# Kernel tuning notes

Hardware: AMD Instinct MI355X
Metric: run time of the kernel (lower is better)

## Reference

```python
import jax, jax.numpy as jnp
import numpy as np

N = 8192
IN_F = 128
OUT_F = 128
ALPHA = 0.2  # LeakyReLU negative slope
NEG_INF = -9e15


def setup_inputs() -> dict:
    key = jax.random.key(0)
    k1, k2, k3, k4 = jax.random.split(key, 4)
    h = jax.random.normal(k1, (N, IN_F), dtype=jnp.float32)
    adj = jax.random.randint(k2, (N, N), 0, 2, dtype=jnp.int32)
    # nn.Linear(in, out, bias=False).weight is (out, in); store as (in, out) for h @ W
    W = jax.random.normal(k3, (IN_F, OUT_F), dtype=jnp.float32) * (1.0 / np.sqrt(IN_F))
    # a: (2*out_features, 1), xavier_uniform with gain=1.414
    limit = 1.414 * np.sqrt(6.0 / (2 * OUT_F + 1))
    a = jax.random.uniform(k4, (2 * OUT_F, 1), dtype=jnp.float32, minval=-limit, maxval=limit)
    return {"h": h, "adj": adj, "W": W, "a": a}


def reference(h, adj, W, a):
    Wh = h @ W  # (N, OUT_F)
    a1 = a[:OUT_F, 0]   # score contribution from source node i
    a2 = a[OUT_F:, 0]   # score contribution from target node j
    # e_ij = leakyrelu(Wh_i . a1 + Wh_j . a2) -- avoids the O(N^2 * 2F) concat
    s1 = Wh @ a1  # (N,)
    s2 = Wh @ a2  # (N,)
    e = jax.nn.leaky_relu(s1[:, None] + s2[None, :], negative_slope=ALPHA)  # (N, N)
    masked = jnp.where(adj > 0, e, NEG_INF)
    attention = jax.nn.softmax(masked, axis=1)  # (N, N)
    # dropout is a no-op in eval mode
    h_prime = attention @ Wh  # (N, OUT_F)
    return jax.nn.elu(h_prime)  # concat=True -> ELU
```

## Files before the change

### kernel.cpp

```cpp
#include <hip/hip_runtime.h>
#include <cstdint>
#include <cstddef>


#define NROW 8192
#define FDIM 128

typedef _Float16 f16;
typedef f16 f16x8 __attribute__((ext_vector_type(8)));
typedef float f32x4 __attribute__((ext_vector_type(4)));
typedef float f32x16 __attribute__((ext_vector_type(16)));

#define WS_WHT 0u
#define WS_BP  (2u*1024u*1024u)
#define WS_S12 (4u*1024u*1024u)
#define WS_RC  (WS_S12 + 64u*1024u)
#define WS_EF  (WS_RC + 128u*1024u)
#define WS_M2  (WS_EF + 64u*1024u)
#define WS_PWS (WS_M2 + 4u*1024u)

__global__ __launch_bounds__(256) void k1_wh(const float* __restrict__ h,
                                             const float* __restrict__ W,
                                             f16* __restrict__ WhT,
                                             f16* __restrict__ Bp,
                                             unsigned* __restrict__ M2key) {
  __shared__ float hT[128 * 36];
  const int t = (int)threadIdx.x;
  const int rb = (int)blockIdx.x * 32;
  if (blockIdx.x == 0 && t == 0) *M2key = 0u;
  const f32x4* hv = (const f32x4*)(h + (size_t)rb * FDIM);
#pragma unroll
  for (int i = 0; i < 4; ++i) {
    int fidx = t + i * 256;
    f32x4 v = hv[fidx];
    int e0 = fidx * 4;
    int r = e0 >> 7, k = e0 & 127;
    hT[(k + 0) * 36 + r] = v[0];
    hT[(k + 1) * 36 + r] = v[1];
    hT[(k + 2) * 36 + r] = v[2];
    hT[(k + 3) * 36 + r] = v[3];
  }
  __syncthreads();
  const int f = t & 127, rh = t >> 7;
  f32x4 z = {0.f, 0.f, 0.f, 0.f};
  f32x4 acc0 = z, acc1 = z, acc2 = z, acc3 = z;
  for (int k = 0; k < 128; ++k) {
    float w = W[k * FDIM + f];
    const f32x4* hp = (const f32x4*)(hT + k * 36 + rh * 16);
    acc0 += hp[0] * w;
    acc1 += hp[1] * w;
    acc2 += hp[2] * w;
    acc3 += hp[3] * w;
  }
  union { f16 hx[16]; uint4 u[2]; } pk;
#pragma unroll
  for (int q = 0; q < 4; ++q) {
    pk.hx[0 + q]  = (f16)acc0[q];
    pk.hx[4 + q]  = (f16)acc1[q];
    pk.hx[8 + q]  = (f16)acc2[q];
    pk.hx[12 + q] = (f16)acc3[q];
  }
  uint4* dst = (uint4*)(WhT + (size_t)f * NROW + rb + rh * 16);
  dst[0] = pk.u[0];
  dst[1] = pk.u[1];
  f16* bdst = Bp + ((size_t)((blockIdx.x * 2 + rh) * 4 + (f >> 5)) * 64 + (f & 31)) * 8;
  *(uint4*)bdst = pk.u[0];
  *(uint4*)(bdst + 256) = pk.u[1];
}

__global__ __launch_bounds__(256) void k1b_s(const f16* __restrict__ WhT,
                                             const float* __restrict__ a,
                                             float2* __restrict__ s12,
                                             unsigned* __restrict__ M2key) {
  __shared__ float part[2][4][64];
  const int l = (int)threadIdx.x & 63;
  const int fc = (int)threadIdx.x >> 6;
  const int r = (int)blockIdx.x * 64 + l;
  float s1 = 0.f, s2 = 0.f;
  for (int f = fc * 32; f < fc * 32 + 32; ++f) {
    float w = (float)WhT[(size_t)f * NROW + r];
    s1 = fmaf(w, a[f], s1);
    s2 = fmaf(w, a[128 + f], s2);
  }
  part[0][fc][l] = s1;
  part[1][fc][l] = s2;
  __syncthreads();
  if (fc == 0) {
    s1 = part[0][0][l] + part[0][1][l] + part[0][2][l] + part[0][3][l];
    s2 = part[1][0][l] + part[1][1][l] + part[1][2][l] + part[1][3][l];
    s12[r] = make_float2(s1, s2);
    float mx = s2;
#pragma unroll
    for (int off = 32; off; off >>= 1) mx = fmaxf(mx, __shfl_xor(mx, off, 64));
    if (l == 0) {
      unsigned key = __float_as_uint(mx);
      key = (key & 0x80000000u) ? ~key : (key | 0x80000000u);
      atomicMax(M2key, key);
    }
  }
}

__global__ __launch_bounds__(256) void k1c_prep(const float2* __restrict__ s12,
                                                const unsigned* __restrict__ M2key,
                                                float4* __restrict__ RC,
                                                float2* __restrict__ EF) {
  int j = (int)blockIdx.x * 256 + (int)threadIdx.x;
  unsigned key = *M2key;
  float M2 = (key & 0x80000000u) ? __uint_as_float(key ^ 0x80000000u)
                                 : __uint_as_float(~key);
  float2 s = s12[j];
  float c = s.x + M2;
  c = fmaxf(c, 0.2f * c);
  RC[j] = make_float4(__expf(-s.x), __expf(s.x - c), __expf(0.2f * s.x - c), 0.f);
  EF[j] = make_float2(__expf(s.y), __expf(0.2f * s.y));
}

__global__ __launch_bounds__(256) void k2_main(const int* __restrict__ adj,
                                               const f16* __restrict__ Bp,
                                               const float4* __restrict__ RC,
                                               const float* __restrict__ EF,
                                               float* __restrict__ Pws,
                                               float* __restrict__ Dws,
                                               int jspan) {
  const int tid = (int)threadIdx.x;
  const int L = tid & 63, w = tid >> 6;
  const int wid = (int)blockIdx.x * 4 + w;
  const int rg = wid & 255;
  const int c = wid >> 8;
  const int rb = rg * 32;
  const int m = L & 31, kb = L >> 5;
  const int row = rb + m;
  const int j0 = c * jspan;
  const int niter = jspan >> 5;

  const float4 rc = RC[row];
  const float tau = rc.x, kap1 = rc.y, kap2 = rc.z;

  const int* ap = adj + (size_t)row * NROW + j0 + kb * 8;
  const f32x4* ep = (const f32x4*)(EF + 2 * (j0 + kb * 8));
  const f16* bp = Bp + (size_t)(j0 >> 4) * 2048 + L * 8;

  int4 A0 = *(const int4*)ap;
  int4 A1 = *(const int4*)(ap + 4);
  int4 A2 = *(const int4*)(ap + 16);
  int4 A3 = *(const int4*)(ap + 20);
  f32x4 E0 = ep[0], E1 = ep[1], E2 = ep[2], E3 = ep[3];
  f32x4 E4 = ep[8], E5 = ep[9], E6 = ep[10], E7 = ep[11];

  f32x16 zz = {0.f};
  f32x16 acc[4] = {zz, zz, zz, zz};
  float dloc = 0.f;

  for (int it = 0; it < niter; ++it) {
    const f16* bt = bp + (size_t)it * 4096;
    f16x8 B00 = *(const f16x8*)(bt);
    f16x8 B01 = *(const f16x8*)(bt + 512);
    f16x8 B02 = *(const f16x8*)(bt + 1024);
    f16x8 B03 = *(const f16x8*)(bt + 1536);
    f16x8 B10 = *(const f16x8*)(bt + 2048);
    f16x8 B11 = *(const f16x8*)(bt + 2560);
    f16x8 B12 = *(const f16x8*)(bt + 3072);
    f16x8 B13 = *(const f16x8*)(bt + 3584);

    f16x8 af0, af1;
    {
      float p;
      p = (E0[0] > tau) ? E0[0] * kap1 : E0[1] * kap2; p = (A0.x > 0) ? p : 0.f; dloc += p; af0[0] = (f16)p;
      p = (E0[2] > tau) ? E0[2] * kap1 : E0[3] * kap2; p = (A0.y > 0) ? p : 0.f; dloc += p; af0[1] = (f16)p;
      p = (E1[0] > tau) ? E1[0] * kap1 : E1[1] * kap2; p = (A0.z > 0) ? p : 0.f; dloc += p; af0[2] = (f16)p;
      p = (E1[2] > tau) ? E1[2] * kap1 : E1[3] * kap2; p = (A0.w > 0) ? p : 0.f; dloc += p; af0[3] = (f16)p;
      p = (E2[0] > tau) ? E2[0] * kap1 : E2[1] * kap2; p = (A1.x > 0) ? p : 0.f; dloc += p; af0[4] = (f16)p;
      p = (E2[2] > tau) ? E2[2] * kap1 : E2[3] * kap2; p = (A1.y > 0) ? p : 0.f; dloc += p; af0[5] = (f16)p;
      p = (E3[0] > tau) ? E3[0] * kap1 : E3[1] * kap2; p = (A1.z > 0) ? p : 0.f; dloc += p; af0[6] = (f16)p;
      p = (E3[2] > tau) ? E3[2] * kap1 : E3[3] * kap2; p = (A1.w > 0) ? p : 0.f; dloc += p; af0[7] = (f16)p;
      p = (E4[0] > tau) ? E4[0] * kap1 : E4[1] * kap2; p = (A2.x > 0) ? p : 0.f; dloc += p; af1[0] = (f16)p;
      p = (E4[2] > tau) ? E4[2] * kap1 : E4[3] * kap2; p = (A2.y > 0) ? p : 0.f; dloc += p; af1[1] = (f16)p;
      p = (E5[0] > tau) ? E5[0] * kap1 : E5[1] * kap2; p = (A2.z > 0) ? p : 0.f; dloc += p; af1[2] = (f16)p;
      p = (E5[2] > tau) ? E5[2] * kap1 : E5[3] * kap2; p = (A2.w > 0) ? p : 0.f; dloc += p; af1[3] = (f16)p;
      p = (E6[0] > tau) ? E6[0] * kap1 : E6[1] * kap2; p = (A3.x > 0) ? p : 0.f; dloc += p; af1[4] = (f16)p;
      p = (E6[2] > tau) ? E6[2] * kap1 : E6[3] * kap2; p = (A3.y > 0) ? p : 0.f; dloc += p; af1[5] = (f16)p;
      p = (E7[0] > tau) ? E7[0] * kap1 : E7[1] * kap2; p = (A3.z > 0) ? p : 0.f; dloc += p; af1[6] = (f16)p;
      p = (E7[2] > tau) ? E7[2] * kap1 : E7[3] * kap2; p = (A3.w > 0) ? p : 0.f; dloc += p; af1[7] = (f16)p;
    }

    int adv = (it < niter - 1) ? 1 : 0;
    ap += adv * 32;
    ep += adv * 16;
    A0 = *(const int4*)ap;
    A1 = *(const int4*)(ap + 4);
    A2 = *(const int4*)(ap + 16);
    A3 = *(const int4*)(ap + 20);
    E0 = ep[0]; E1 = ep[1]; E2 = ep[2]; E3 = ep[3];
    E4 = ep[8]; E5 = ep[9]; E6 = ep[10]; E7 = ep[11];

    acc[0] = __builtin_amdgcn_mfma_f32_32x32x16_f16(af0, B00, acc[0], 0, 0, 0);
    acc[1] = __builtin_amdgcn_mfma_f32_32x32x16_f16(af0, B01, acc[1], 0, 0, 0);
    acc[2] = __builtin_amdgcn_mfma_f32_32x32x16_f16(af0, B02, acc[2], 0, 0, 0);
    acc[3] = __builtin_amdgcn_mfma_f32_32x32x16_f16(af0, B03, acc[3], 0, 0, 0);
    acc[0] = __builtin_amdgcn_mfma_f32_32x32x16_f16(af1, B10, acc[0], 0, 0, 0);
    acc[1] = __builtin_amdgcn_mfma_f32_32x32x16_f16(af1, B11, acc[1], 0, 0, 0);
    acc[2] = __builtin_amdgcn_mfma_f32_32x32x16_f16(af1, B12, acc[2], 0, 0, 0);
    acc[3] = __builtin_amdgcn_mfma_f32_32x32x16_f16(af1, B13, acc[3], 0, 0, 0);
  }

  dloc += __shfl_xor(dloc, 32, 64);
  if (L < 32) Dws[(size_t)c * NROW + row] = dloc;

  float* P = Pws + ((size_t)c * NROW + rb) * FDIM + (L & 31);
#pragma unroll
  for (int nt = 0; nt < 4; ++nt) {
#pragma unroll
    for (int reg = 0; reg < 16; ++reg) {
      int rr = (reg & 3) + 8 * (reg >> 2) + 4 * kb;
      P[(size_t)rr * FDIM + nt * 32] = acc[nt][reg];
    }
  }
}

__global__ __launch_bounds__(256) void k3_comb(const float* __restrict__ Pws,
                                               const float* __restrict__ Dws,
                                               float* __restrict__ out, int S) {
  int g = (int)blockIdx.x * 256 + (int)threadIdx.x;
  int r = g >> 5, f4 = g & 31;
  f32x4 s = {0.f, 0.f, 0.f, 0.f};
  float den = 0.f;
  for (int c2 = 0; c2 < S; ++c2) {
    s += *(const f32x4*)(Pws + ((size_t)c2 * NROW + r) * FDIM + f4 * 4);
    den += Dws[(size_t)c2 * NROW + r];
  }
  float inv = 1.0f / den;
  f32x4 o;
#pragma unroll
  for (int e = 0; e < 4; ++e) {
    float x = s[e] * inv;
    o[e] = x > 0.f ? x : expm1f(x);
  }
  *(f32x4*)(out + (size_t)r * FDIM + f4 * 4) = o;
}

extern "C" void kernel_launch(void* const* d_in, const int* in_sizes, int n_in,
                              void* d_out, int out_size, void* d_ws, size_t ws_size,
                              hipStream_t stream) {
  const float* h = (const float*)d_in[0];
  const int* adj = (const int*)d_in[1];
  const float* W = (const float*)d_in[2];
  const float* a = (const float*)d_in[3];
  float* out = (float*)d_out;
  char* ws = (char*)d_ws;
  f16* WhT = (f16*)(ws + WS_WHT);
  f16* Bp = (f16*)(ws + WS_BP);
  float2* s12 = (float2*)(ws + WS_S12);
  float4* RC = (float4*)(ws + WS_RC);
  float2* EF = (float2*)(ws + WS_EF);
  unsigned* M2 = (unsigned*)(ws + WS_M2);

  const size_t partial_bytes = (size_t)NROW * FDIM * 4;
  int S = (ws_size >= WS_PWS + 8 * partial_bytes + 8 * NROW * 4) ? 8 : 2;
  float* Pws = (float*)(ws + WS_PWS);
  float* Dws = (float*)(ws + WS_PWS + (size_t)S * partial_bytes);
  int jspan = NROW / S;

  k1_wh<<<dim3(256), dim3(256), 0, stream>>>(h, W, WhT, Bp, M2);
  k1b_s<<<dim3(128), dim3(256), 0, stream>>>(WhT, a, s12, M2);
  k1c_prep<<<dim3(32), dim3(256), 0, stream>>>(s12, M2, RC, EF);
  k2_main<<<dim3(64 * S), dim3(256), 0, stream>>>(adj, Bp, RC, (const float*)EF, Pws, Dws, jspan);
  k3_comb<<<dim3(1024), dim3(256), 0, stream>>>(Pws, Dws, out, S);
}
```

Before: 449.8 us.

## Switch attention GEMM to 16x16x32 MFMA tiles with deeper adjacency prefetch

The main kernel now gives each wave 16 rows instead of 32 and uses 16x16x32 MFMA, so twice as many waves run and there are more in flight to hide the adjacency stream from HBM. The Wh operand layout written by k1_wh is changed to match the new fragment shape. Adjacency loads are prefetched four iterations ahead to raise memory-level parallelism. The LeakyReLU branch on tau is replaced by fmaxf of the two exponential products, which removes the tau table. The cost is that each B fragment is now reused over only 16 rows, which doubles B traffic from L2.

```diff
diff --git a/kernel.cpp b/kernel.cpp
--- a/kernel.cpp
+++ b/kernel.cpp
@@ -9,13 +9,12 @@
 typedef _Float16 f16;
 typedef f16 f16x8 __attribute__((ext_vector_type(8)));
 typedef float f32x4 __attribute__((ext_vector_type(4)));
-typedef float f32x16 __attribute__((ext_vector_type(16)));
 
 #define WS_WHT 0u
 #define WS_BP  (2u*1024u*1024u)
 #define WS_S12 (4u*1024u*1024u)
-#define WS_RC  (WS_S12 + 64u*1024u)
-#define WS_EF  (WS_RC + 128u*1024u)
+#define WS_K12 (WS_S12 + 64u*1024u)
+#define WS_EF  (WS_K12 + 64u*1024u)
 #define WS_M2  (WS_EF + 64u*1024u)
 #define WS_PWS (WS_M2 + 4u*1024u)
 
@@ -63,9 +62,10 @@
   uint4* dst = (uint4*)(WhT + (size_t)f * NROW + rb + rh * 16);
   dst[0] = pk.u[0];
   dst[1] = pk.u[1];
-  f16* bdst = Bp + ((size_t)((blockIdx.x * 2 + rh) * 4 + (f >> 5)) * 64 + (f & 31)) * 8;
+  f16* bdst = Bp + (size_t)blockIdx.x * 4096 + (size_t)(f >> 4) * 512
+                 + (size_t)(2 * rh) * 128 + (size_t)(f & 15) * 8;
   *(uint4*)bdst = pk.u[0];
-  *(uint4*)(bdst + 256) = pk.u[1];
+  *(uint4*)(bdst + 128) = pk.u[1];
 }
 
 __global__ __launch_bounds__(256) void k1b_s(const f16* __restrict__ WhT,
@@ -102,7 +102,7 @@
 
 __global__ __launch_bounds__(256) void k1c_prep(const float2* __restrict__ s12,
                                                 const unsigned* __restrict__ M2key,
-                                                float4* __restrict__ RC,
+                                                float2* __restrict__ K12,
                                                 float2* __restrict__ EF) {
   int j = (int)blockIdx.x * 256 + (int)threadIdx.x;
   unsigned key = *M2key;
@@ -111,13 +111,13 @@
   float2 s = s12[j];
   float c = s.x + M2;
   c = fmaxf(c, 0.2f * c);
-  RC[j] = make_float4(__expf(-s.x), __expf(s.x - c), __expf(0.2f * s.x - c), 0.f);
+  K12[j] = make_float2(__expf(s.x - c), __expf(0.2f * s.x - c));
   EF[j] = make_float2(__expf(s.y), __expf(0.2f * s.y));
 }
 
 __global__ __launch_bounds__(256) void k2_main(const int* __restrict__ adj,
                                                const f16* __restrict__ Bp,
-                                               const float4* __restrict__ RC,
+                                               const float2* __restrict__ K12,
                                                const float* __restrict__ EF,
                                                float* __restrict__ Pws,
                                                float* __restrict__ Dws,
@@ -125,94 +125,96 @@
   const int tid = (int)threadIdx.x;
   const int L = tid & 63, w = tid >> 6;
   const int wid = (int)blockIdx.x * 4 + w;
-  const int rg = wid & 255;
-  const int c = wid >> 8;
-  const int rb = rg * 32;
-  const int m = L & 31, kb = L >> 5;
+  const int rg = wid & 511;
+  const int c = wid >> 9;
+  const int rb = rg * 16;
+  const int m = L & 15, kq = L >> 4;
   const int row = rb + m;
   const int j0 = c * jspan;
   const int niter = jspan >> 5;
 
-  const float4 rc = RC[row];
-  const float tau = rc.x, kap1 = rc.y, kap2 = rc.z;
-
-  const int* ap = adj + (size_t)row * NROW + j0 + kb * 8;
-  const f32x4* ep = (const f32x4*)(EF + 2 * (j0 + kb * 8));
-  const f16* bp = Bp + (size_t)(j0 >> 4) * 2048 + L * 8;
-
-  int4 A0 = *(const int4*)ap;
-  int4 A1 = *(const int4*)(ap + 4);
-  int4 A2 = *(const int4*)(ap + 16);
-  int4 A3 = *(const int4*)(ap + 20);
-  f32x4 E0 = ep[0], E1 = ep[1], E2 = ep[2], E3 = ep[3];
-  f32x4 E4 = ep[8], E5 = ep[9], E6 = ep[10], E7 = ep[11];
-
-  f32x16 zz = {0.f};
-  f32x16 acc[4] = {zz, zz, zz, zz};
+  const float2 kk = K12[row];
+  const float kap1 = kk.x, kap2 = kk.y;
+
+  const int* ap = adj + (size_t)row * NROW + j0 + kq * 8;
+  const float* ep = EF ? (EF + 2 * (size_t)(j0 + kq * 8)) : EF;
+  const f16* bp = Bp + (size_t)(j0 >> 5) * 4096 + (size_t)L * 8;
+
+  int4 A[4][2];
+#pragma unroll
+  for (int s = 0; s < 4; ++s) {
+    A[s][0] = *(const int4*)(ap + s * 32);
+    A[s][1] = *(const int4*)(ap + s * 32 + 4);
+  }
+  f32x4 E[4];
+#pragma unroll
+  for (int q = 0; q < 4; ++q) E[q] = *(const f32x4*)(ep + q * 4);
+
+  f32x4 z = {0.f, 0.f, 0.f, 0.f};
+  f32x4 acc[8] = {z, z, z, z, z, z, z, z};
   float dloc = 0.f;
 
-  for (int it = 0; it < niter; ++it) {
-    const f16* bt = bp + (size_t)it * 4096;
-    f16x8 B00 = *(const f16x8*)(bt);
-    f16x8 B01 = *(const f16x8*)(bt + 512);
-    f16x8 B02 = *(const f16x8*)(bt + 1024);
-    f16x8 B03 = *(const f16x8*)(bt + 1536);
-    f16x8 B10 = *(const f16x8*)(bt + 2048);
-    f16x8 B11 = *(const f16x8*)(bt + 2560);
-    f16x8 B12 = *(const f16x8*)(bt + 3072);
-    f16x8 B13 = *(const f16x8*)(bt + 3584);
-
-    f16x8 af0, af1;
-    {
-      float p;
-      p = (E0[0] > tau) ? E0[0] * kap1 : E0[1] * kap2; p = (A0.x > 0) ? p : 0.f; dloc += p; af0[0] = (f16)p;
-      p = (E0[2] > tau) ? E0[2] * kap1 : E0[3] * kap2; p = (A0.y > 0) ? p : 0.f; dloc += p; af0[1] = (f16)p;
-      p = (E1[0] > tau) ? E1[0] * kap1 : E1[1] * kap2; p = (A0.z > 0) ? p : 0.f; dloc += p; af0[2] = (f16)p;
-      p = (E1[2] > tau) ? E1[2] * kap1 : E1[3] * kap2; p = (A0.w > 0) ? p : 0.f; dloc += p; af0[3] = (f16)p;
-      p = (E2[0] > tau) ? E2[0] * kap1 : E2[1] * kap2; p = (A1.x > 0) ? p : 0.f; dloc += p; af0[4] = (f16)p;
-      p = (E2[2] > tau) ? E2[2] * kap1 : E2[3] * kap2; p = (A1.y > 0) ? p : 0.f; dloc += p; af0[5] = (f16)p;
-      p = (E3[0] > tau) ? E3[0] * kap1 : E3[1] * kap2; p = (A1.z > 0) ? p : 0.f; dloc += p; af0[6] = (f16)p;
-      p = (E3[2] > tau) ? E3[2] * kap1 : E3[3] * kap2; p = (A1.w > 0) ? p : 0.f; dloc += p; af0[7] = (f16)p;
-      p = (E4[0] > tau) ? E4[0] * kap1 : E4[1] * kap2; p = (A2.x > 0) ? p : 0.f; dloc += p; af1[0] = (f16)p;
-      p = (E4[2] > tau) ? E4[2] * kap1 : E4[3] * kap2; p = (A2.y > 0) ? p : 0.f; dloc += p; af1[1] = (f16)p;
-      p = (E5[0] > tau) ? E5[0] * kap1 : E5[1] * kap2; p = (A2.z > 0) ? p : 0.f; dloc += p; af1[2] = (f16)p;
-      p = (E5[2] > tau) ? E5[2] * kap1 : E5[3] * kap2; p = (A2.w > 0) ? p : 0.f; dloc += p; af1[3] = (f16)p;
-      p = (E6[0] > tau) ? E6[0] * kap1 : E6[1] * kap2; p = (A3.x > 0) ? p : 0.f; dloc += p; af1[4] = (f16)p;
-      p = (E6[2] > tau) ? E6[2] * kap1 : E6[3] * kap2; p = (A3.y > 0) ? p : 0.f; dloc += p; af1[5] = (f16)p;
-      p = (E7[0] > tau) ? E7[0] * kap1 : E7[1] * kap2; p = (A3.z > 0) ? p : 0.f; dloc += p; af1[6] = (f16)p;
-      p = (E7[2] > tau) ? E7[2] * kap1 : E7[3] * kap2; p = (A3.w > 0) ? p : 0.f; dloc += p; af1[7] = (f16)p;
+  for (int ii = 0; ii < niter; ii += 4) {
+#pragma unroll
+    for (int s = 0; s < 4; ++s) {
+      const int it = ii + s;
+      const f16* bt = bp + (size_t)it * 4096;
+      f16x8 B0 = *(const f16x8*)(bt);
+      f16x8 B1 = *(const f16x8*)(bt + 512);
+      f16x8 B2 = *(const f16x8*)(bt + 1024);
+      f16x8 B3 = *(const f16x8*)(bt + 1536);
+      f16x8 B4 = *(const f16x8*)(bt + 2048);
+      f16x8 B5 = *(const f16x8*)(bt + 2560);
+      f16x8 B6 = *(const f16x8*)(bt + 3072);
+      f16x8 B7 = *(const f16x8*)(bt + 3584);
+
+      f16x8 af;
+      {
+        const int4 a0 = A[s][0], a1 = A[s][1];
+        float p;
+        p = fmaxf(E[0][0] * kap1, E[0][1] * kap2); p = (a0.x > 0) ? p : 0.f; dloc += p; af[0] = (f16)p;
+        p = fmaxf(E[0][2] * kap1, E[0][3] * kap2); p = (a0.y > 0) ? p : 0.f; dloc += p; af[1] = (f16)p;
+        p = fmaxf(E[1][0] * kap1, E[1][1] * kap2); p = (a0.z > 0) ? p : 0.f; dloc += p; af[2] = (f16)p;
+        p = fmaxf(E[1][2] * kap1, E[1][3] * kap2); p = (a0.w > 0) ? p : 0.f; dloc += p; af[3] = (f16)p;
+        p = fmaxf(E[2][0] * kap1, E[2][1] * kap2); p = (a1.x > 0) ? p : 0.f; dloc += p; af[4] = (f16)p;
+        p = fmaxf(E[2][2] * kap1, E[2][3] * kap2); p = (a1.y > 0) ? p : 0.f; dloc += p; af[5] = (f16)p;
+        p = fmaxf(E[3][0] * kap1, E[3][1] * kap2); p = (a1.z > 0) ? p : 0.f; dloc += p; af[6] = (f16)p;
+        p = fmaxf(E[3][2] * kap1, E[3][3] * kap2); p = (a1.w > 0) ? p : 0.f; dloc += p; af[7] = (f16)p;
+      }
+
+      {
+        const int itn = (it + 4 < niter) ? it + 4 : it;
+        A[s][0] = *(const int4*)(ap + itn * 32);
+        A[s][1] = *(const int4*)(ap + itn * 32 + 4);
+      }
+      {
+        const int itn = (it + 1 < niter) ? it + 1 : it;
+#pragma unroll
+        for (int q = 0; q < 4; ++q) E[q] = *(const f32x4*)(ep + itn * 64 + q * 4);
+      }
+
+      acc[0] = __builtin_amdgcn_mfma_f32_16x16x32_f16(af, B0, acc[0], 0, 0, 0);
+      acc[1] = __builtin_amdgcn_mfma_f32_16x16x32_f16(af, B1, acc[1], 0, 0, 0);
+      acc[2] = __builtin_amdgcn_mfma_f32_16x16x32_f16(af, B2, acc[2], 0, 0, 0);
+      acc[3] = __builtin_amdgcn_mfma_f32_16x16x32_f16(af, B3, acc[3], 0, 0, 0);
+      acc[4] = __builtin_amdgcn_mfma_f32_16x16x32_f16(af, B4, acc[4], 0, 0, 0);
+      acc[5] = __builtin_amdgcn_mfma_f32_16x16x32_f16(af, B5, acc[5], 0, 0, 0);
+      acc[6] = __builtin_amdgcn_mfma_f32_16x16x32_f16(af, B6, acc[6], 0, 0, 0);
+      acc[7] = __builtin_amdgcn_mfma_f32_16x16x32_f16(af, B7, acc[7], 0, 0, 0);
     }
-
-    int adv = (it < niter - 1) ? 1 : 0;
-    ap += adv * 32;
-    ep += adv * 16;
-    A0 = *(const int4*)ap;
-    A1 = *(const int4*)(ap + 4);
-    A2 = *(const int4*)(ap + 16);
-    A3 = *(const int4*)(ap + 20);
-    E0 = ep[0]; E1 = ep[1]; E2 = ep[2]; E3 = ep[3];
-    E4 = ep[8]; E5 = ep[9]; E6 = ep[10]; E7 = ep[11];
-
-    acc[0] = __builtin_amdgcn_mfma_f32_32x32x16_f16(af0, B00, acc[0], 0, 0, 0);
-    acc[1] = __builtin_amdgcn_mfma_f32_32x32x16_f16(af0, B01, acc[1], 0, 0, 0);
-    acc[2] = __builtin_amdgcn_mfma_f32_32x32x16_f16(af0, B02, acc[2], 0, 0, 0);
-    acc[3] = __builtin_amdgcn_mfma_f32_32x32x16_f16(af0, B03, acc[3], 0, 0, 0);
-    acc[0] = __builtin_amdgcn_mfma_f32_32x32x16_f16(af1, B10, acc[0], 0, 0, 0);
-    acc[1] = __builtin_amdgcn_mfma_f32_32x32x16_f16(af1, B11, acc[1], 0, 0, 0);
-    acc[2] = __builtin_amdgcn_mfma_f32_32x32x16_f16(af1, B12, acc[2], 0, 0, 0);
-    acc[3] = __builtin_amdgcn_mfma_f32_32x32x16_f16(af1, B13, acc[3], 0, 0, 0);
-  }
-
+  }
+
+  dloc += __shfl_xor(dloc, 16, 64);
   dloc += __shfl_xor(dloc, 32, 64);
-  if (L < 32) Dws[(size_t)c * NROW + row] = dloc;
-
-  float* P = Pws + ((size_t)c * NROW + rb) * FDIM + (L & 31);
-#pragma unroll
-  for (int nt = 0; nt < 4; ++nt) {
-#pragma unroll
-    for (int reg = 0; reg < 16; ++reg) {
-      int rr = (reg & 3) + 8 * (reg >> 2) + 4 * kb;
-      P[(size_t)rr * FDIM + nt * 32] = acc[nt][reg];
+  if (L < 16) Dws[(size_t)c * NROW + rb + L] = dloc;
+
+  float* P = Pws + ((size_t)c * NROW + rb) * FDIM + (L & 15);
+#pragma unroll
+  for (int nt = 0; nt < 8; ++nt) {
+#pragma unroll
+    for (int reg = 0; reg < 4; ++reg) {
+      int rr = kq * 4 + reg;
+      P[(size_t)rr * FDIM + nt * 16] = acc[nt][reg];
     }
   }
 }
@@ -250,7 +252,7 @@
   f16* WhT = (f16*)(ws + WS_WHT);
   f16* Bp = (f16*)(ws + WS_BP);
   float2* s12 = (float2*)(ws + WS_S12);
-  float4* RC = (float4*)(ws + WS_RC);
+  float2* K12 = (float2*)(ws + WS_K12);
   float2* EF = (float2*)(ws + WS_EF);
   unsigned* M2 = (unsigned*)(ws + WS_M2);
 
@@ -262,7 +264,7 @@
 
   k1_wh<<<dim3(256), dim3(256), 0, stream>>>(h, W, WhT, Bp, M2);
   k1b_s<<<dim3(128), dim3(256), 0, stream>>>(WhT, a, s12, M2);
-  k1c_prep<<<dim3(32), dim3(256), 0, stream>>>(s12, M2, RC, EF);
-  k2_main<<<dim3(64 * S), dim3(256), 0, stream>>>(adj, Bp, RC, (const float*)EF, Pws, Dws, jspan);
+  k1c_prep<<<dim3(32), dim3(256), 0, stream>>>(s12, M2, K12, EF);
+  k2_main<<<dim3(128 * S), dim3(256), 0, stream>>>(adj, Bp, K12, (const float*)EF, Pws, Dws, jspan);
   k3_comb<<<dim3(1024), dim3(256), 0, stream>>>(Pws, Dws, out, S);
 }
```

New measurement: 477.2 us. 1.06x slower.
